# Optimization experiments

Measured on AMD Instinct MI355X. Metric: run time of the kernel, lower is better.

The kernel has to match this reference:

```python
import jax, jax.numpy as jnp
import numpy as np

D = 256          # in_dim == out_dim for both layers
B, S = 8, 1024   # batch, seq_len
EPS = 1e-5       # LayerNorm eps (torch default)


def _layernorm(x, g, b):
    mu = jnp.mean(x, axis=-1, keepdims=True)
    var = jnp.var(x, axis=-1, keepdims=True)
    return (x - mu) * jax.lax.rsqrt(var + EPS) * g + b


def _periods(d):
    i = jnp.arange(d, dtype=jnp.float32)
    # periods[i, j] = i*d + j + 2
    return i[:, None] * d + i[None, :] + 2.0


def _layer(x, M, P, g, b, positions):
    # x: [B, S, in_dim] -> [B, S, out_dim]
    x_trans = jnp.einsum('bsj,ij->bsi', x, M)      # x @ M.T
    x_trans = _layernorm(x_trans, g, b)
    k = positions.astype(jnp.float32)[:, None, None]            # [S,1,1]
    phi = jnp.cos(2.0 * jnp.pi * k / _periods(D)[None])         # [S,D,D]
    Mk = P[None] * phi                                          # [S,D,D]
    Nk = jnp.einsum('bsj,sij->bsi', x_trans, Mk)
    # use_residual='separate' with in_dim==out_dim -> Identity residual
    return Nk + x


def setup_inputs() -> dict:
    key = jax.random.key(0)
    ks = jax.random.split(key, 5)
    seq = jax.random.normal(ks[0], (B, S, D), dtype=jnp.float32)
    M1 = jax.random.uniform(ks[1], (D, D), jnp.float32, -0.5, 0.5)
    P1 = jax.random.uniform(ks[2], (D, D), jnp.float32, -0.1, 0.1)
    M2 = jax.random.uniform(ks[3], (D, D), jnp.float32, -0.5, 0.5)
    P2 = jax.random.uniform(ks[4], (D, D), jnp.float32, -0.1, 0.1)
    g1 = jnp.ones((D,), jnp.float32); b1 = jnp.zeros((D,), jnp.float32)
    g2 = jnp.ones((D,), jnp.float32); b2 = jnp.zeros((D,), jnp.float32)
    return {"seq": seq, "M1": M1, "P1": P1, "g1": g1, "b1": b1,
            "M2": M2, "P2": P2, "g2": g2, "b2": b2}


def reference(seq, M1, P1, g1, b1, M2, P2, g2, b2):
    positions = jnp.arange(S)
    x = _layer(seq, M1, P1, g1, b1, positions)
    x = _layer(x, M2, P2, g2, b2, positions)
    return x
```

## Files before the change

### kernel.cpp

```cpp
#include <hip/hip_runtime.h>

#define DD 256
#define BB 8
#define SS 1024
#define XSTRIDE 264
#define RSTRIDE 132

#define LAYER_BYTES 262144
#define PTAB_OFF    131072
#define Y1_OFF      (2 * LAYER_BYTES)
#define Y1_BYTES    (BB * SS * DD * 4)
#define WS_NEEDED   (Y1_OFF + Y1_BYTES)

typedef _Float16 half8  __attribute__((ext_vector_type(8)));
typedef _Float16 half2t __attribute__((ext_vector_type(2)));
typedef __fp16   fp16x2 __attribute__((ext_vector_type(2)));
typedef __attribute__((ext_vector_type(4))) float float4v;

union h8u { half8 h; half2t h2[4]; };

__device__ __forceinline__ half2t pkrtz(float a, float b) {
    union { fp16x2 f; half2t h; } cv;
    cv.f = __builtin_amdgcn_cvt_pkrtz(a, b);
    return cv.h;
}

__device__ __forceinline__ float cosrev(float x) {
    return __builtin_amdgcn_cosf(__builtin_amdgcn_fractf(x));
}

__global__ void build_tabs(const float* __restrict__ M1, const float* __restrict__ P1,
                           const float* __restrict__ M2, const float* __restrict__ P2,
                           char* __restrict__ ws)
{
    int gid   = blockIdx.x * 256 + threadIdx.x;
    int layer = gid >> 13;
    int gi    = gid & 8191;
    int idx   = gi >> 6;
    int lane  = gi & 63;
    int wt    = idx & 15;
    int l15   = lane & 15, quad = lane >> 4;
    int kt    = idx >> 4;
    int n     = 16 * wt + l15;
    int j0    = kt * 32 + quad * 8;

    const float* Msrc = layer ? M2 : M1;
    const float* Psrc = layer ? P2 : P1;

    h8u mh, ph;
    #pragma unroll
    for (int e = 0; e < 4; ++e) {
        float ma = Msrc[(size_t)n * DD + j0 + 2 * e];
        float mb = Msrc[(size_t)n * DD + j0 + 2 * e + 1];
        float pa = Psrc[(size_t)n * DD + j0 + 2 * e];
        float pb = Psrc[(size_t)n * DD + j0 + 2 * e + 1];
        mh.h2[e] = pkrtz(ma, mb);
        ph.h2[e] = pkrtz(pa, pb);
    }
    char* base = ws + (size_t)layer * LAYER_BYTES;
    ((half8*)base)[gi]              = mh.h;
    ((half8*)(base + PTAB_OFF))[gi] = ph.h;
}

__global__ __launch_bounds__(512, 8)
void split_layer(const float* __restrict__ src,
                 const char*  __restrict__ lbase,
                 const float* __restrict__ g,
                 const float* __restrict__ be,
                 float* __restrict__ dst)
{
    __shared__ __align__(16) _Float16 xsb[16][XSTRIDE];
    __shared__ __align__(16) _Float16 xtb[16][XSTRIDE];
    __shared__ __align__(16) float2 stats[16][8];
    __shared__ __align__(16) float res_lds[16][RSTRIDE];

    const half8* Mtab = (const half8*)lbase;
    const half8* Ptab = (const half8*)(lbase + PTAB_OFF);

    const int tid  = threadIdx.x;
    const int w    = tid >> 6;
    const int lane = tid & 63;
    const int l15  = lane & 15;
    const int quad = lane >> 4;
    const int sp   = blockIdx.x >> 1;
    const int ch   = blockIdx.x & 1;
    const int s0   = sp * 2;
    const float k0 = (float)s0;

    {
        const float4* src4 = (const float4*)src;
        #pragma unroll
        for (int u = 0; u < 2; ++u) {
            int v  = tid + 512 * u;
            int sl = v >> 9;
            int rm = v & 511;
            int b  = rm >> 6, j4 = rm & 63;
            float4 x = src4[((size_t)b * SS + s0 + sl) * 64 + j4];
            int r = sl * 8 + b;
            half2t* d2 = (half2t*)&xsb[r][4 * j4];
            d2[0] = pkrtz(x.x, x.y);
            d2[1] = pkrtz(x.z, x.w);
            if ((j4 >> 5) == ch)
                *(float4*)&res_lds[r][4 * (j4 & 31)] = x;
        }
    }
    __syncthreads();

    float4v acc1[2];
    acc1[0] = (float4v){0.f, 0.f, 0.f, 0.f};
    acc1[1] = (float4v){0.f, 0.f, 0.f, 0.f};

    half8 aN  = *(const half8*)&xsb[l15][quad * 8];
    half8 b0N = Mtab[(2 * w) * 64 + lane];
    half8 b1N = Mtab[(2 * w + 1) * 64 + lane];
    #pragma unroll 1
    for (int kt = 0; kt < 8; ++kt) {
        half8 aC = aN, b0C = b0N, b1C = b1N;
        if (kt < 7) {
            aN  = *(const half8*)&xsb[l15][(kt + 1) * 32 + quad * 8];
            b0N = Mtab[((kt + 1) * 16 + 2 * w) * 64 + lane];
            b1N = Mtab[((kt + 1) * 16 + 2 * w + 1) * 64 + lane];
        }
        acc1[0] = __builtin_amdgcn_mfma_f32_16x16x32_f16(aC, b0C, acc1[0], 0, 0, 0);
        acc1[1] = __builtin_amdgcn_mfma_f32_16x16x32_f16(aC, b1C, acc1[1], 0, 0, 0);
    }

    half8 pN = Ptab[(ch * 8 + w) * 64 + lane];

    #pragma unroll
    for (int reg = 0; reg < 4; ++reg) {
        float v0 = acc1[0][reg], v1 = acc1[1][reg];
        float sm = v0 + v1;
        float sq = fmaf(v0, v0, v1 * v1);
        #pragma unroll
        for (int off = 1; off < 16; off <<= 1) {
            sm += __shfl_xor(sm, off, 64);
            sq += __shfl_xor(sq, off, 64);
        }
        if (l15 == 0) stats[quad * 4 + reg][w] = make_float2(sm, sq);
    }
    __syncthreads();
    {
        int c0i = 16 * (2 * w) + l15, c1i = 16 * (2 * w + 1) + l15;
        float gv0 = g[c0i], bv0 = be[c0i];
        float gv1 = g[c1i], bv1 = be[c1i];
        #pragma unroll
        for (int reg = 0; reg < 4; ++reg) {
            int m = quad * 4 + reg;
            const float4* s4 = (const float4*)&stats[m][0];
            float4 q0 = s4[0], q1 = s4[1], q2 = s4[2], q3 = s4[3];
            float sm = (q0.x + q0.z) + (q1.x + q1.z) + (q2.x + q2.z) + (q3.x + q3.z);
            float sq = (q0.y + q0.w) + (q1.y + q1.w) + (q2.y + q2.w) + (q3.y + q3.w);
            float mm = sm * (1.f / DD);
            float rs = rsqrtf(sq * (1.f / DD) - mm * mm + 1e-5f);
            xtb[m][c0i] = (_Float16)fmaf((acc1[0][reg] - mm) * rs, gv0, bv0);
            xtb[m][c1i] = (_Float16)fmaf((acc1[1][reg] - mm) * rs, gv1, bv1);
        }
    }
    __syncthreads();

    float4v accS[2];
    accS[0] = (float4v){0.f, 0.f, 0.f, 0.f};
    accS[1] = (float4v){0.f, 0.f, 0.f, 0.f};

    const int nB = 16 * (ch * 8 + w) + l15;
    float fb = (float)(nB * DD + quad * 8 + 2);
    half8 aBN = *(const half8*)&xtb[l15][quad * 8];

    #pragma unroll 1
    for (int kt = 0; kt < 8; ++kt) {
        half8 aC = aBN;
        h8u pC; pC.h = pN;
        if (kt < 7) {
            aBN = *(const half8*)&xtb[l15][(kt + 1) * 32 + quad * 8];
            pN  = Ptab[((kt + 1) * 16 + ch * 8 + w) * 64 + lane];
        }
        h8u bA, bB;
        #pragma unroll
        for (int e = 0; e < 4; ++e) {
            float ia = __builtin_amdgcn_rcpf(fb + (float)(2 * e));
            float ib = __builtin_amdgcn_rcpf(fb + (float)(2 * e + 1));
            float a0 = k0 * ia, b0f = k0 * ib;
            float a1 = a0 + ia, b1f = b0f + ib;
            half2t c0 = pkrtz(cosrev(a0), cosrev(b0f));
            half2t c1 = pkrtz(cosrev(a1), cosrev(b1f));
            bA.h2[e] = pC.h2[e] * c0;
            bB.h2[e] = pC.h2[e] * c1;
        }
        accS[0] = __builtin_amdgcn_mfma_f32_16x16x32_f16(aC, bA.h, accS[0], 0, 0, 0);
        accS[1] = __builtin_amdgcn_mfma_f32_16x16x32_f16(aC, bB.h, accS[1], 0, 0, 0);
        fb += 32.0f;
    }

    {
        int col = nB;
        int cl  = 16 * w + l15;
        float4v av = (quad < 2) ? accS[0] : accS[1];
        int sl = quad >> 1;
        #pragma unroll
        for (int reg = 0; reg < 4; ++reg) {
            int m = quad * 4 + reg;
            int b = m & 7;
            dst[((size_t)b * SS + s0 + sl) * DD + col] = av[reg] + res_lds[m][cl];
        }
    }
}

__global__ __launch_bounds__(512, 4)
void fused_fallback(const float* __restrict__ seq,
                    const float* __restrict__ M1, const float* __restrict__ P1,
                    const float* __restrict__ g1, const float* __restrict__ be1,
                    const float* __restrict__ M2, const float* __restrict__ P2,
                    const float* __restrict__ g2, const float* __restrict__ be2,
                    float* __restrict__ out)
{
    __shared__ __align__(16) _Float16 xsb[16][XSTRIDE];
    __shared__ __align__(16) _Float16 xtb[16][XSTRIDE];
    __shared__ __align__(16) float2 stats[16][8];
    __shared__ __align__(16) float res_lds[16][2 * RSTRIDE];

    const int tid  = threadIdx.x;
    const int w    = tid >> 6;
    const int lane = tid & 63;
    const int l15  = lane & 15;
    const int quad = lane >> 4;
    const int s0   = blockIdx.x * 2;
    const float k0 = (float)s0;

    {
        const float4* seq4 = (const float4*)seq;
        #pragma unroll
        for (int u = 0; u < 2; ++u) {
            int v  = tid + 512 * u;
            int sl = v >> 9;
            int rm = v & 511;
            int b  = rm >> 6, j4 = rm & 63;
            float4 x = seq4[((size_t)b * SS + s0 + sl) * 64 + j4];
            int r = sl * 8 + b;
            half2t* d2 = (half2t*)&xsb[r][4 * j4];
            d2[0] = pkrtz(x.x, x.y);
            d2[1] = pkrtz(x.z, x.w);
            *(float4*)&res_lds[r][4 * j4] = x;
        }
    }
    __syncthreads();

    #pragma unroll 1
    for (int layer = 0; layer < 2; ++layer) {
        const float* M  = layer ? M2  : M1;
        const float* P  = layer ? P2  : P1;
        const float* g  = layer ? g2  : g1;
        const float* be = layer ? be2 : be1;

        float4v acc1[2];
        acc1[0] = (float4v){0.f, 0.f, 0.f, 0.f};
        acc1[1] = (float4v){0.f, 0.f, 0.f, 0.f};

        #pragma unroll 1
        for (int kt = 0; kt < 8; ++kt) {
            half8 a = *(const half8*)&xsb[l15][kt * 32 + quad * 8];
            #pragma unroll
            for (int t = 0; t < 2; ++t) {
                int n = 16 * (2 * w + t) + l15;
                const float4* Mr = (const float4*)M + ((size_t)n * 64 + kt * 8 + quad * 2);
                float4 m0 = Mr[0], m1 = Mr[1];
                h8u bb2;
                bb2.h2[0] = pkrtz(m0.x, m0.y);
                bb2.h2[1] = pkrtz(m0.z, m0.w);
                bb2.h2[2] = pkrtz(m1.x, m1.y);
                bb2.h2[3] = pkrtz(m1.z, m1.w);
                acc1[t] = __builtin_amdgcn_mfma_f32_16x16x32_f16(a, bb2.h, acc1[t], 0, 0, 0);
            }
        }

        #pragma unroll
        for (int reg = 0; reg < 4; ++reg) {
            float v0 = acc1[0][reg], v1 = acc1[1][reg];
            float sm = v0 + v1;
            float sq = fmaf(v0, v0, v1 * v1);
            #pragma unroll
            for (int off = 1; off < 16; off <<= 1) {
                sm += __shfl_xor(sm, off, 64);
                sq += __shfl_xor(sq, off, 64);
            }
            if (l15 == 0) stats[quad * 4 + reg][w] = make_float2(sm, sq);
        }
        __syncthreads();
        {
            int c0i = 16 * (2 * w) + l15, c1i = 16 * (2 * w + 1) + l15;
            float gv0 = g[c0i], bv0 = be[c0i];
            float gv1 = g[c1i], bv1 = be[c1i];
            #pragma unroll
            for (int reg = 0; reg < 4; ++reg) {
                int m = quad * 4 + reg;
                const float4* s4 = (const float4*)&stats[m][0];
                float4 q0 = s4[0], q1 = s4[1], q2 = s4[2], q3 = s4[3];
                float sm = (q0.x + q0.z) + (q1.x + q1.z) + (q2.x + q2.z) + (q3.x + q3.z);
                float sq = (q0.y + q0.w) + (q1.y + q1.w) + (q2.y + q2.w) + (q3.y + q3.w);
                float mm = sm * (1.f / DD);
                float rs = rsqrtf(sq * (1.f / DD) - mm * mm + 1e-5f);
                xtb[m][c0i] = (_Float16)fmaf((acc1[0][reg] - mm) * rs, gv0, bv0);
                xtb[m][c1i] = (_Float16)fmaf((acc1[1][reg] - mm) * rs, gv1, bv1);
            }
        }
        __syncthreads();

        float4v accS[2][2];
        #pragma unroll
        for (int k = 0; k < 2; ++k)
            #pragma unroll
            for (int t = 0; t < 2; ++t) accS[k][t] = (float4v){0.f, 0.f, 0.f, 0.f};

        float fb0 = (float)((16 * (2 * w) + l15) * DD + quad * 8 + 2);
        float fb1 = fb0 + 16.0f * DD;

        #pragma unroll 1
        for (int kt = 0; kt < 8; ++kt) {
            half8 a = *(const half8*)&xtb[l15][kt * 32 + quad * 8];
            #pragma unroll
            for (int t = 0; t < 2; ++t) {
                int n = 16 * (2 * w + t) + l15;
                const float4* Pr = (const float4*)P + ((size_t)n * 64 + kt * 8 + quad * 2);
                float4 p0 = Pr[0], p1 = Pr[1];
                h8u pv;
                pv.h2[0] = pkrtz(p0.x, p0.y);
                pv.h2[1] = pkrtz(p0.z, p0.w);
                pv.h2[2] = pkrtz(p1.x, p1.y);
                pv.h2[3] = pkrtz(p1.z, p1.w);
                float fb = (t == 0) ? fb0 : fb1;
                h8u bA, bB;
                #pragma unroll
                for (int e = 0; e < 4; ++e) {
                    float ia = __builtin_amdgcn_rcpf(fb + (float)(2 * e));
                    float ib = __builtin_amdgcn_rcpf(fb + (float)(2 * e + 1));
                    float a0 = k0 * ia, b0f = k0 * ib;
                    float a1 = a0 + ia, b1f = b0f + ib;
                    half2t c0 = pkrtz(cosrev(a0), cosrev(b0f));
                    half2t c1 = pkrtz(cosrev(a1), cosrev(b1f));
                    bA.h2[e] = pv.h2[e] * c0;
                    bB.h2[e] = pv.h2[e] * c1;
                }
                accS[0][t] = __builtin_amdgcn_mfma_f32_16x16x32_f16(a, bA.h, accS[0][t], 0, 0, 0);
                accS[1][t] = __builtin_amdgcn_mfma_f32_16x16x32_f16(a, bB.h, accS[1][t], 0, 0, 0);
            }
            fb0 += 32.0f; fb1 += 32.0f;
        }

        #pragma unroll
        for (int t = 0; t < 2; ++t) {
            int col = 16 * (2 * w + t) + l15;
            float4v av = (quad < 2) ? accS[0][t] : accS[1][t];
            int sl = quad >> 1;
            #pragma unroll
            for (int reg = 0; reg < 4; ++reg) {
                int m = quad * 4 + reg;
                int b = m & 7;
                float val = av[reg] + res_lds[m][col];
                if (layer == 0) {
                    res_lds[m][col] = val;
                    xsb[m][col] = (_Float16)val;
                } else {
                    out[((size_t)b * SS + s0 + sl) * DD + col] = val;
                }
            }
        }
        if (layer == 0) __syncthreads();
    }
}

extern "C" void kernel_launch(void* const* d_in, const int* in_sizes, int n_in,
                              void* d_out, int out_size, void* d_ws, size_t ws_size,
                              hipStream_t stream)
{
    const float* seq = (const float*)d_in[0];
    const float* M1  = (const float*)d_in[1];
    const float* P1  = (const float*)d_in[2];
    const float* g1  = (const float*)d_in[3];
    const float* b1  = (const float*)d_in[4];
    const float* M2  = (const float*)d_in[5];
    const float* P2  = (const float*)d_in[6];
    const float* g2  = (const float*)d_in[7];
    const float* b2  = (const float*)d_in[8];
    float* out = (float*)d_out;

    if (ws_size >= WS_NEEDED) {
        char* ws = (char*)d_ws;
        float* y1 = (float*)(ws + Y1_OFF);
        build_tabs<<<64, 256, 0, stream>>>(M1, P1, M2, P2, ws);
        split_layer<<<SS, 512, 0, stream>>>(seq, ws, g1, b1, y1);
        split_layer<<<SS, 512, 0, stream>>>(y1, ws + LAYER_BYTES, g2, b2, out);
    } else {
        fused_fallback<<<SS / 2, 512, 0, stream>>>(
            seq, M1, P1, g1, b1, M2, P2, g2, b2, out);
    }
}
```

Before: 127.6 us.

## Split each layer into LayerNorm-GEMM and modulated-GEMM kernels, drop redundant fract

Each layer now runs as two kernels. phase_a computes x@M.T and the LayerNorm once per sequence pair and writes the fp16 result to workspace. phase_b reads it back and runs the cosine-modulated GEMM across four 256-thread blocks per sequence pair. Before, two blocks each recomputed the full first GEMM and LayerNorm. For column tiles other than the first, the cosine argument is always below one revolution, so the fractf range reduction is skipped there. The price is two extra kernel launches, a global round-trip of the fp16 intermediate, and the residual read from global memory instead of LDS.

Measured after the change: 129.0 us. About the same (+1.0%).

```diff
diff --git a/kernel.cpp b/kernel.cpp
--- a/kernel.cpp
+++ b/kernel.cpp
@@ -4,11 +4,12 @@
 #define BB 8
 #define SS 1024
 #define XSTRIDE 264
-#define RSTRIDE 132
 
 #define LAYER_BYTES 262144
 #define PTAB_OFF    131072
-#define Y1_OFF      (2 * LAYER_BYTES)
+#define XT_OFF      (2 * LAYER_BYTES)
+#define XT_BYTES    (BB * SS * DD * 2)
+#define Y1_OFF      (XT_OFF + XT_BYTES)
 #define Y1_BYTES    (BB * SS * DD * 4)
 #define WS_NEEDED   (Y1_OFF + Y1_BYTES)
 
@@ -27,6 +28,9 @@
 
 __device__ __forceinline__ float cosrev(float x) {
     return __builtin_amdgcn_cosf(__builtin_amdgcn_fractf(x));
+}
+__device__ __forceinline__ float cosq(float x) {
+    return __builtin_amdgcn_cosf(x);
 }
 
 __global__ void build_tabs(const float* __restrict__ M1, const float* __restrict__ P1,
@@ -62,30 +66,25 @@
     ((half8*)(base + PTAB_OFF))[gi] = ph.h;
 }
 
-__global__ __launch_bounds__(512, 8)
-void split_layer(const float* __restrict__ src,
-                 const char*  __restrict__ lbase,
-                 const float* __restrict__ g,
-                 const float* __restrict__ be,
-                 float* __restrict__ dst)
+__global__ __launch_bounds__(512, 4)
+void phase_a(const float* __restrict__ src,
+             const char*  __restrict__ lbase,
+             const float* __restrict__ g,
+             const float* __restrict__ be,
+             _Float16* __restrict__ xt)
 {
     __shared__ __align__(16) _Float16 xsb[16][XSTRIDE];
     __shared__ __align__(16) _Float16 xtb[16][XSTRIDE];
     __shared__ __align__(16) float2 stats[16][8];
-    __shared__ __align__(16) float res_lds[16][RSTRIDE];
 
     const half8* Mtab = (const half8*)lbase;
-    const half8* Ptab = (const half8*)(lbase + PTAB_OFF);
 
     const int tid  = threadIdx.x;
     const int w    = tid >> 6;
     const int lane = tid & 63;
     const int l15  = lane & 15;
     const int quad = lane >> 4;
-    const int sp   = blockIdx.x >> 1;
-    const int ch   = blockIdx.x & 1;
-    const int s0   = sp * 2;
-    const float k0 = (float)s0;
+    const int s0   = blockIdx.x * 2;
 
     {
         const float4* src4 = (const float4*)src;
@@ -96,12 +95,9 @@
             int rm = v & 511;
             int b  = rm >> 6, j4 = rm & 63;
             float4 x = src4[((size_t)b * SS + s0 + sl) * 64 + j4];
-            int r = sl * 8 + b;
-            half2t* d2 = (half2t*)&xsb[r][4 * j4];
-            d2[0] = pkrtz(x.x, x.y);
-            d2[1] = pkrtz(x.z, x.w);
-            if ((j4 >> 5) == ch)
-                *(float4*)&res_lds[r][4 * (j4 & 31)] = x;
+            half2t* dst = (half2t*)&xsb[sl * 8 + b][4 * j4];
+            dst[0] = pkrtz(x.x, x.y);
+            dst[1] = pkrtz(x.z, x.w);
         }
     }
     __syncthreads();
@@ -125,8 +121,6 @@
         acc1[1] = __builtin_amdgcn_mfma_f32_16x16x32_f16(aC, b1C, acc1[1], 0, 0, 0);
     }
 
-    half8 pN = Ptab[(ch * 8 + w) * 64 + lane];
-
     #pragma unroll
     for (int reg = 0; reg < 4; ++reg) {
         float v0 = acc1[0][reg], v1 = acc1[1][reg];
@@ -159,33 +153,89 @@
     }
     __syncthreads();
 
+    {
+        int row = tid >> 5, c16 = tid & 31;
+        int b = row & 7, sl = row >> 3;
+        float4 v = *(const float4*)&xtb[row][c16 * 8];
+        *(float4*)&xt[((size_t)b * SS + s0 + sl) * DD + c16 * 8] = v;
+    }
+}
+
+__global__ __launch_bounds__(256, 8)
+void phase_b(const _Float16* __restrict__ xt,
+             const char*  __restrict__ lbase,
+             const float* __restrict__ res,
+             float* __restrict__ dst)
+{
+    __shared__ __align__(16) _Float16 xtb[16][XSTRIDE];
+
+    const half8* Ptab = (const half8*)(lbase + PTAB_OFF);
+
+    const int tid  = threadIdx.x;
+    const int w    = tid >> 6;
+    const int lane = tid & 63;
+    const int l15  = lane & 15;
+    const int quad = lane >> 4;
+    const int sp   = blockIdx.x >> 2;
+    const int nq   = blockIdx.x & 3;
+    const int s0   = sp * 2;
+    const float k0 = (float)s0;
+    const int ntile = nq * 4 + w;
+
+    {
+        const float4* xt4 = (const float4*)xt;
+        #pragma unroll
+        for (int u = 0; u < 2; ++u) {
+            int f = tid + 256 * u;
+            int row = f >> 5, c = f & 31;
+            int b = row & 7, sl = row >> 3;
+            float4 v = xt4[((size_t)b * SS + s0 + sl) * 32 + c];
+            *(float4*)&xtb[row][c * 8] = v;
+        }
+    }
+    __syncthreads();
+
     float4v accS[2];
     accS[0] = (float4v){0.f, 0.f, 0.f, 0.f};
     accS[1] = (float4v){0.f, 0.f, 0.f, 0.f};
 
-    const int nB = 16 * (ch * 8 + w) + l15;
-    float fb = (float)(nB * DD + quad * 8 + 2);
-    half8 aBN = *(const half8*)&xtb[l15][quad * 8];
+    float fb = (float)((16 * ntile + l15) * DD + quad * 8 + 2);
+    half8 aN = *(const half8*)&xtb[l15][quad * 8];
+    half8 pN = Ptab[ntile * 64 + lane];
 
     #pragma unroll 1
     for (int kt = 0; kt < 8; ++kt) {
-        half8 aC = aBN;
+        half8 aC = aN;
         h8u pC; pC.h = pN;
         if (kt < 7) {
-            aBN = *(const half8*)&xtb[l15][(kt + 1) * 32 + quad * 8];
-            pN  = Ptab[((kt + 1) * 16 + ch * 8 + w) * 64 + lane];
+            aN = *(const half8*)&xtb[l15][(kt + 1) * 32 + quad * 8];
+            pN = Ptab[((kt + 1) * 16 + ntile) * 64 + lane];
         }
         h8u bA, bB;
-        #pragma unroll
-        for (int e = 0; e < 4; ++e) {
-            float ia = __builtin_amdgcn_rcpf(fb + (float)(2 * e));
-            float ib = __builtin_amdgcn_rcpf(fb + (float)(2 * e + 1));
-            float a0 = k0 * ia, b0f = k0 * ib;
-            float a1 = a0 + ia, b1f = b0f + ib;
-            half2t c0 = pkrtz(cosrev(a0), cosrev(b0f));
-            half2t c1 = pkrtz(cosrev(a1), cosrev(b1f));
-            bA.h2[e] = pC.h2[e] * c0;
-            bB.h2[e] = pC.h2[e] * c1;
+        if (ntile == 0) {
+            #pragma unroll
+            for (int e = 0; e < 4; ++e) {
+                float ia = __builtin_amdgcn_rcpf(fb + (float)(2 * e));
+                float ib = __builtin_amdgcn_rcpf(fb + (float)(2 * e + 1));
+                float a0 = k0 * ia, b0f = k0 * ib;
+                float a1 = a0 + ia, b1f = b0f + ib;
+                half2t c0 = pkrtz(cosrev(a0), cosrev(b0f));
+                half2t c1 = pkrtz(cosrev(a1), cosrev(b1f));
+                bA.h2[e] = pC.h2[e] * c0;
+                bB.h2[e] = pC.h2[e] * c1;
+            }
+        } else {
+            #pragma unroll
+            for (int e = 0; e < 4; ++e) {
+                float ia = __builtin_amdgcn_rcpf(fb + (float)(2 * e));
+                float ib = __builtin_amdgcn_rcpf(fb + (float)(2 * e + 1));
+                float a0 = k0 * ia, b0f = k0 * ib;
+                float a1 = a0 + ia, b1f = b0f + ib;
+                half2t c0 = pkrtz(cosq(a0), cosq(b0f));
+                half2t c1 = pkrtz(cosq(a1), cosq(b1f));
+                bA.h2[e] = pC.h2[e] * c0;
+                bB.h2[e] = pC.h2[e] * c1;
+            }
         }
         accS[0] = __builtin_amdgcn_mfma_f32_16x16x32_f16(aC, bA.h, accS[0], 0, 0, 0);
         accS[1] = __builtin_amdgcn_mfma_f32_16x16x32_f16(aC, bB.h, accS[1], 0, 0, 0);
@@ -193,15 +243,14 @@
     }
 
     {
-        int col = nB;
-        int cl  = 16 * w + l15;
+        int col = 16 * ntile + l15;
         float4v av = (quad < 2) ? accS[0] : accS[1];
-        int sl = quad >> 1;
         #pragma unroll
         for (int reg = 0; reg < 4; ++reg) {
             int m = quad * 4 + reg;
-            int b = m & 7;
-            dst[((size_t)b * SS + s0 + sl) * DD + col] = av[reg] + res_lds[m][cl];
+            int b = m & 7, sl = m >> 3;
+            size_t idx = ((size_t)b * SS + s0 + sl) * DD + col;
+            dst[idx] = av[reg] + res[idx];
         }
     }
 }
@@ -217,7 +266,7 @@
     __shared__ __align__(16) _Float16 xsb[16][XSTRIDE];
     __shared__ __align__(16) _Float16 xtb[16][XSTRIDE];
     __shared__ __align__(16) float2 stats[16][8];
-    __shared__ __align__(16) float res_lds[16][2 * RSTRIDE];
+    __shared__ __align__(16) float res_lds[16][260];
 
     const int tid  = threadIdx.x;
     const int w    = tid >> 6;
@@ -385,10 +434,13 @@
 
     if (ws_size >= WS_NEEDED) {
         char* ws = (char*)d_ws;
-        float* y1 = (float*)(ws + Y1_OFF);
+        _Float16* xt = (_Float16*)(ws + XT_OFF);
+        float*    y1 = (float*)(ws + Y1_OFF);
         build_tabs<<<64, 256, 0, stream>>>(M1, P1, M2, P2, ws);
-        split_layer<<<SS, 512, 0, stream>>>(seq, ws, g1, b1, y1);
-        split_layer<<<SS, 512, 0, stream>>>(y1, ws + LAYER_BYTES, g2, b2, out);
+        phase_a<<<SS / 2, 512, 0, stream>>>(seq, ws, g1, b1, xt);
+        phase_b<<<2 * SS, 256, 0, stream>>>(xt, ws, seq, y1);
+        phase_a<<<SS / 2, 512, 0, stream>>>(y1, ws + LAYER_BYTES, g2, b2, xt);
+        phase_b<<<2 * SS, 256, 0, stream>>>(xt, ws + LAYER_BYTES, y1, out);
     } else {
         fused_fallback<<<SS / 2, 512, 0, stream>>>(
             seq, M1, P1, g1, b1, M2, P2, g2, b2, out);
```
